# Kernel tuning notes

Measured on AMD Instinct MI355X. Metric: run time of the kernel, lower is better.

The kernel has to match this reference:

```python
import jax, jax.numpy as jnp
import numpy as np

B, AT, NBR = 8, 96, 512
NG, NT = 25, 5            # n_gaussian_triple, n_theta
NANG = NG * NT            # 125, filternet input dim
NF = 128                  # n_filters
NB = 128                  # n_atom_basis


def ssp(x):
    # shifted softplus: ln(0.5*e^x + 0.5) = softplus(x) - ln(2)
    return jax.nn.softplus(x) - jnp.asarray(np.log(2.0), x.dtype)


def setup_inputs() -> dict:
    key = jax.random.key(0)
    ks = jax.random.split(key, 16)
    s = lambda fan_in: 1.0 / np.sqrt(fan_in)
    return {
        "x": jax.random.normal(ks[0], (B, AT, NB), jnp.float32),
        "triple_ijk": jax.random.uniform(ks[1], (B, AT, NBR, NANG), jnp.float32),
        "neighbors_j": jax.random.randint(ks[2], (B, AT, NBR), 0, AT, jnp.int32),
        "neighbors_k": jax.random.randint(ks[3], (B, AT, NBR), 0, AT, jnp.int32),
        "triple_mask": jnp.ones((B, AT, NBR), jnp.float32),
        # filter network (Dense ssp -> Dense linear)
        "W1": jax.random.normal(ks[4], (NANG, NF), jnp.float32) * s(NANG),
        "b1": jnp.zeros((NF,), jnp.float32),
        "W2": jax.random.normal(ks[5], (NF, NF), jnp.float32) * s(NF),
        "b2": jnp.zeros((NF,), jnp.float32),
        # cfconv in2f (no bias) and f2out (ssp activation)
        "Win": jax.random.normal(ks[6], (NB, NF), jnp.float32) * s(NB),
        "Wf2": jax.random.normal(ks[7], (NF, NB), jnp.float32) * s(NF),
        "bf2": jnp.zeros((NB,), jnp.float32),
        # final dense (linear) before residual
        "Wd": jax.random.normal(ks[8], (NB, NB), jnp.float32) * s(NB),
        "bd": jnp.zeros((NB,), jnp.float32),
    }


def _gather_atoms(y, nbh):
    # y: (B, At, F); nbh: (B, At, Nbr) -> (B, At, Nbr, F)
    b, at, nbr = nbh.shape
    idx = nbh.reshape(b, at * nbr, 1)
    return jnp.take_along_axis(y, idx, axis=1).reshape(b, at, nbr, y.shape[-1])


def reference(x, triple_ijk, neighbors_j, neighbors_k, triple_mask,
              W1, b1, W2, b2, Win, Wf2, bf2, Wd, bd):
    # filter network on angular/radial triple features -> (B, At, Nbr, NF)
    W_triple = ssp(triple_ijk @ W1 + b1) @ W2 + b2
    # in2f
    y = x @ Win                                  # (B, At, NF)
    y_j = _gather_atoms(y, neighbors_j)          # (B, At, Nbr, NF)
    y_k = _gather_atoms(y, neighbors_k)          # (B, At, Nbr, NF)
    # element-wise continuous-filter conv over triples, mask padded triples
    yt = y_j * y_k * W_triple * triple_mask[..., None]
    agg = jnp.sum(yt, axis=2)                    # sum-aggregate over triples
    v = ssp(agg @ Wf2 + bf2)                     # f2out with shifted softplus
    v = v @ Wd + bd                              # interaction dense
    return x + v                                 # residual
```

## Files before the change

### kernel.cpp

```cpp
#include <hip/hip_runtime.h>
#include <math.h>

#define B_    8
#define AT_   96
#define NBR_  512
#define NANG_ 125
#define NF_   128
#define NB_   128
#define TN    32
#define NCHUNK 4
#define CROWS (NBR_ / NCHUNK)
#define TSTRIDE 136
#define JSTRIDE 132

typedef __attribute__((ext_vector_type(8))) short bf16x8;
typedef __attribute__((ext_vector_type(4))) float f32x4;
typedef float f32x4u __attribute__((ext_vector_type(4), aligned(4)));
typedef __attribute__((ext_vector_type(4))) unsigned int u32x4;

__device__ __forceinline__ short f2bf(float f) {
    union { float f; unsigned u; } x; x.f = f;
    return (short)((x.u + 0x8000u) >> 16);
}

__device__ __forceinline__ unsigned pk2bf(float a, float b) {
    union { float f; unsigned u; } x, y; x.f = a; y.f = b;
    return ((x.u + 0x8000u) >> 16) | ((y.u + 0x8000u) & 0xffff0000u);
}

__device__ __forceinline__ float sspf(float x) {
    float p = __builtin_amdgcn_exp2f(x * 1.44269504088896340736f);
    float l = __builtin_amdgcn_logf(1.0f + p);
    return 0.69314718055994530942f * l - 0.69314718055994530942f;
}

__global__ __launch_bounds__(128) void prep_kernel(
    const float* __restrict__ x, const float* __restrict__ Win,
    const float* __restrict__ W1, const float* __restrict__ W2,
    float* __restrict__ y, short* __restrict__ w1p, short* __restrict__ w2p)
{
    __shared__ float xs[4][NB_];
    int blk = blockIdx.x, tid = threadIdx.x;
    if (blk < 192) {
        int row0 = blk * 4;
        #pragma unroll
        for (int r = 0; r < 4; r++) xs[r][tid] = x[(row0 + r) * NB_ + tid];
        __syncthreads();
        float a0 = 0.f, a1 = 0.f, a2 = 0.f, a3 = 0.f;
        #pragma unroll 8
        for (int k = 0; k < NB_; k++) {
            float w = Win[k * NF_ + tid];
            a0 = fmaf(xs[0][k], w, a0);
            a1 = fmaf(xs[1][k], w, a1);
            a2 = fmaf(xs[2][k], w, a2);
            a3 = fmaf(xs[3][k], w, a3);
        }
        y[(row0 + 0) * NF_ + tid] = a0;
        y[(row0 + 1) * NF_ + tid] = a1;
        y[(row0 + 2) * NF_ + tid] = a2;
        y[(row0 + 3) * NF_ + tid] = a3;
    } else {
        int t = (blk - 192) * 128 + tid;
        int j = t & 7, lane = (t >> 3) & 63, ks = (t >> 9) & 3, ct = t >> 11;
        int k = ks * 32 + (lane >> 4) * 8 + j;
        int n = ct * 16 + (lane & 15);
        w1p[t] = (k < NANG_) ? f2bf(W1[k * NF_ + n]) : (short)0;
        w2p[t] = f2bf(W2[k * NF_ + n]);
    }
}

__global__ __launch_bounds__(256) void triple_partial(
    const float* __restrict__ trip,
    const int* __restrict__ nbj, const int* __restrict__ nbk,
    const float* __restrict__ maskg,
    const float* __restrict__ b1g, const float* __restrict__ b2g,
    const float* __restrict__ y, const short* __restrict__ w1p,
    const short* __restrict__ w2p, float* __restrict__ pagg)
{
    __shared__ short ts[TN * TSTRIDE];
    __shared__ short hs[TN * TSTRIDE];
    __shared__ float yjk[TN * JSTRIDE];

    const int tid = threadIdx.x;
    const int wave = tid >> 6, lane = tid & 63;
    const int quad = lane >> 4, col = lane & 15;
    const int blk = blockIdx.x;
    const int bid = blk >> 2, c = blk & 3;
    const int b = bid / AT_;

    const float* tpc = trip + (long)bid * NBR_ * NANG_ + (long)c * CROWS * NANG_;
    const int nb_base = bid * NBR_ + c * CROWS;

    const int ct0 = 2 * wave, ct1 = 2 * wave + 1;
    const int f0 = ct0 * 16 + col, f1 = ct1 * 16 + col;
    const float bias1_0 = b1g[f0], bias1_1 = b1g[f1];
    const float bias2_0 = b2g[f0], bias2_1 = b2g[f1];

    const int srow = tid >> 3, schunk = tid & 7;
    const int yrow = tid >> 3, ypart = tid & 7;

    bf16x8 w1f0[4], w1f1[4];
    #pragma unroll
    for (int ks = 0; ks < 4; ks++) {
        w1f0[ks] = *(const bf16x8*)&w1p[(ct0 * 4 + ks) * 512 + lane * 8];
        w1f1[ks] = *(const bf16x8*)&w1p[(ct1 * 4 + ks) * 512 + lane * 8];
    }

    float accw0 = 0.f, accw1 = 0.f;

    for (int nt = 0; nt < CROWS / TN; nt++) {
        const float* tp = tpc + nt * TN * NANG_;
        const int nrow0 = nb_base + nt * TN;

        const float* rowp = tp + srow * NANG_ + schunk * 16;
        f32x4u v0, v1, v2, v3;
        if (schunk < 7) {
            v0 = *(const f32x4u*)(rowp + 0);
            v1 = *(const f32x4u*)(rowp + 4);
            v2 = *(const f32x4u*)(rowp + 8);
            v3 = *(const f32x4u*)(rowp + 12);
        } else {
            v0 = *(const f32x4u*)(rowp + 0);
            v1 = *(const f32x4u*)(rowp + 4);
            v2 = *(const f32x4u*)(rowp + 8);
            v3.x = rowp[12]; v3.y = 0.f; v3.z = 0.f; v3.w = 0.f;
        }

        const int jj = nbj[nrow0 + yrow], kk = nbk[nrow0 + yrow];
        const float m = maskg[nrow0 + yrow];
        const float* yjp = y + (b * AT_ + jj) * NF_ + ypart * 16;
        const float* ykp = y + (b * AT_ + kk) * NF_ + ypart * 16;
        f32x4 j0 = ((const f32x4*)yjp)[0], j1 = ((const f32x4*)yjp)[1];
        f32x4 j2 = ((const f32x4*)yjp)[2], j3 = ((const f32x4*)yjp)[3];
        f32x4 k0 = ((const f32x4*)ykp)[0], k1 = ((const f32x4*)ykp)[1];
        f32x4 k2 = ((const f32x4*)ykp)[2], k3 = ((const f32x4*)ykp)[3];

        __syncthreads();

        {
            u32x4 pA, pB;
            pA.x = pk2bf(v0.x, v0.y); pA.y = pk2bf(v0.z, v0.w);
            pA.z = pk2bf(v1.x, v1.y); pA.w = pk2bf(v1.z, v1.w);
            pB.x = pk2bf(v2.x, v2.y); pB.y = pk2bf(v2.z, v2.w);
            pB.z = pk2bf(v3.x, v3.y); pB.w = pk2bf(v3.z, v3.w);
            u32x4* dst = (u32x4*)&ts[srow * TSTRIDE + schunk * 16];
            dst[0] = pA;
            dst[1] = pB;
        }
        {
            float* d = &yjk[yrow * JSTRIDE + ypart * 16];
            *(f32x4*)(d + 0)  = j0 * k0 * m;
            *(f32x4*)(d + 4)  = j1 * k1 * m;
            *(f32x4*)(d + 8)  = j2 * k2 * m;
            *(f32x4*)(d + 12) = j3 * k3 * m;
        }
        __syncthreads();

        f32x4 d00 = {0,0,0,0}, d01 = {0,0,0,0}, d10 = {0,0,0,0}, d11 = {0,0,0,0};
        #pragma unroll
        for (int ks = 0; ks < 4; ks++) {
            bf16x8 a0 = *(const bf16x8*)&ts[(     col) * TSTRIDE + ks * 32 + quad * 8];
            bf16x8 a1 = *(const bf16x8*)&ts[(16 + col) * TSTRIDE + ks * 32 + quad * 8];
            d00 = __builtin_amdgcn_mfma_f32_16x16x32_bf16(a0, w1f0[ks], d00, 0, 0, 0);
            d01 = __builtin_amdgcn_mfma_f32_16x16x32_bf16(a0, w1f1[ks], d01, 0, 0, 0);
            d10 = __builtin_amdgcn_mfma_f32_16x16x32_bf16(a1, w1f0[ks], d10, 0, 0, 0);
            d11 = __builtin_amdgcn_mfma_f32_16x16x32_bf16(a1, w1f1[ks], d11, 0, 0, 0);
        }
        #pragma unroll
        for (int r = 0; r < 4; r++) {
            int row0 = quad * 4 + r, row1 = 16 + quad * 4 + r;
            hs[row0 * TSTRIDE + f0] = f2bf(sspf(d00[r] + bias1_0));
            hs[row0 * TSTRIDE + f1] = f2bf(sspf(d01[r] + bias1_1));
            hs[row1 * TSTRIDE + f0] = f2bf(sspf(d10[r] + bias1_0));
            hs[row1 * TSTRIDE + f1] = f2bf(sspf(d11[r] + bias1_1));
        }
        __syncthreads();

        f32x4 e00 = {0,0,0,0}, e01 = {0,0,0,0}, e10 = {0,0,0,0}, e11 = {0,0,0,0};
        #pragma unroll
        for (int ks = 0; ks < 4; ks++) {
            bf16x8 a0 = *(const bf16x8*)&hs[(     col) * TSTRIDE + ks * 32 + quad * 8];
            bf16x8 a1 = *(const bf16x8*)&hs[(16 + col) * TSTRIDE + ks * 32 + quad * 8];
            bf16x8 w0 = *(const bf16x8*)&w2p[(ct0 * 4 + ks) * 512 + lane * 8];
            bf16x8 w1 = *(const bf16x8*)&w2p[(ct1 * 4 + ks) * 512 + lane * 8];
            e00 = __builtin_amdgcn_mfma_f32_16x16x32_bf16(a0, w0, e00, 0, 0, 0);
            e01 = __builtin_amdgcn_mfma_f32_16x16x32_bf16(a0, w1, e01, 0, 0, 0);
            e10 = __builtin_amdgcn_mfma_f32_16x16x32_bf16(a1, w0, e10, 0, 0, 0);
            e11 = __builtin_amdgcn_mfma_f32_16x16x32_bf16(a1, w1, e11, 0, 0, 0);
        }
        #pragma unroll
        for (int r = 0; r < 4; r++) {
            int row0 = quad * 4 + r, row1 = 16 + quad * 4 + r;
            accw0 += (e00[r] + bias2_0) * yjk[row0 * JSTRIDE + f0];
            accw1 += (e01[r] + bias2_1) * yjk[row0 * JSTRIDE + f1];
            accw0 += (e10[r] + bias2_0) * yjk[row1 * JSTRIDE + f0];
            accw1 += (e11[r] + bias2_1) * yjk[row1 * JSTRIDE + f1];
        }
    }

    accw0 += __shfl_xor(accw0, 16, 64);
    accw0 += __shfl_xor(accw0, 32, 64);
    accw1 += __shfl_xor(accw1, 16, 64);
    accw1 += __shfl_xor(accw1, 32, 64);
    if (quad == 0) {
        pagg[blk * NF_ + f0] = accw0;
        pagg[blk * NF_ + f1] = accw1;
    }
}

__global__ __launch_bounds__(128) void finish_kernel(
    const float* __restrict__ x, const float* __restrict__ pagg,
    const float* __restrict__ Wf2, const float* __restrict__ bf2,
    const float* __restrict__ Wd, const float* __restrict__ bd,
    float* __restrict__ out)
{
    __shared__ float aggs[NF_];
    __shared__ float t1s[NF_];
    int bid = blockIdx.x, f = threadIdx.x;
    float a = pagg[(bid * 4 + 0) * NF_ + f] + pagg[(bid * 4 + 1) * NF_ + f]
            + pagg[(bid * 4 + 2) * NF_ + f] + pagg[(bid * 4 + 3) * NF_ + f];
    aggs[f] = a;
    __syncthreads();
    float acc = 0.f;
    #pragma unroll 8
    for (int k = 0; k < NF_; k++) acc = fmaf(aggs[k], Wf2[k * NB_ + f], acc);
    t1s[f] = sspf(acc + bf2[f]);
    __syncthreads();
    acc = 0.f;
    #pragma unroll 8
    for (int k = 0; k < NB_; k++) acc = fmaf(t1s[k], Wd[k * NB_ + f], acc);
    out[bid * NB_ + f] = x[bid * NB_ + f] + acc + bd[f];
}

extern "C" void kernel_launch(void* const* d_in, const int* in_sizes, int n_in,
                              void* d_out, int out_size, void* d_ws, size_t ws_size,
                              hipStream_t stream) {
    const float* x    = (const float*)d_in[0];
    const float* trip = (const float*)d_in[1];
    const int*   nbj  = (const int*)d_in[2];
    const int*   nbk  = (const int*)d_in[3];
    const float* mask = (const float*)d_in[4];
    const float* W1   = (const float*)d_in[5];
    const float* b1   = (const float*)d_in[6];
    const float* W2   = (const float*)d_in[7];
    const float* b2   = (const float*)d_in[8];
    const float* Win  = (const float*)d_in[9];
    const float* Wf2  = (const float*)d_in[10];
    const float* bf2  = (const float*)d_in[11];
    const float* Wd   = (const float*)d_in[12];
    const float* bd   = (const float*)d_in[13];
    float* out = (float*)d_out;

    char* ws = (char*)d_ws;
    float* y    = (float*)ws;
    short* w1p  = (short*)(ws + 393216);
    short* w2p  = (short*)(ws + 393216 + 32768);
    float* pagg = (float*)(ws + 393216 + 65536);

    prep_kernel<<<320, 128, 0, stream>>>(x, Win, W1, W2, y, w1p, w2p);
    triple_partial<<<B_ * AT_ * NCHUNK, 256, 0, stream>>>(trip, nbj, nbk, mask,
        b1, b2, y, w1p, w2p, pagg);
    finish_kernel<<<B_ * AT_, 128, 0, stream>>>(x, pagg, Wf2, bf2, Wd, bd, out);
}
```

Baseline: 352.6 us.

## Split triples into 8 chunks, keep W2 fragments in registers, store yjk as bf16

Doubles the number of blocks by splitting each atom's 512 triples into 8 chunks instead of 4, which gives more parallelism across CUs. The W2 MFMA fragments are loaded into registers once instead of being re-read from global memory every tile. The yj*yk*mask product is stored in shared memory as bf16, which cuts LDS footprint so more blocks can be resident. In exchange the kernel uses more registers, the final reduction has more partials to sum, and the bf16 rounding of the gather product costs some precision.

```diff
diff --git a/kernel.cpp b/kernel.cpp
--- a/kernel.cpp
+++ b/kernel.cpp
@@ -8,10 +8,9 @@
 #define NF_   128
 #define NB_   128
 #define TN    32
-#define NCHUNK 4
+#define NCHUNK 8
 #define CROWS (NBR_ / NCHUNK)
 #define TSTRIDE 136
-#define JSTRIDE 132
 
 typedef __attribute__((ext_vector_type(8))) short bf16x8;
 typedef __attribute__((ext_vector_type(4))) float f32x4;
@@ -22,7 +21,10 @@
     union { float f; unsigned u; } x; x.f = f;
     return (short)((x.u + 0x8000u) >> 16);
 }
-
+__device__ __forceinline__ float bf2f(unsigned short h) {
+    union { unsigned u; float f; } x; x.u = ((unsigned)h) << 16;
+    return x.f;
+}
 __device__ __forceinline__ unsigned pk2bf(float a, float b) {
     union { float f; unsigned u; } x, y; x.f = a; y.f = b;
     return ((x.u + 0x8000u) >> 16) | ((y.u + 0x8000u) & 0xffff0000u);
@@ -79,13 +81,13 @@
 {
     __shared__ short ts[TN * TSTRIDE];
     __shared__ short hs[TN * TSTRIDE];
-    __shared__ float yjk[TN * JSTRIDE];
+    __shared__ unsigned short yjkb[TN * TSTRIDE];
 
     const int tid = threadIdx.x;
     const int wave = tid >> 6, lane = tid & 63;
     const int quad = lane >> 4, col = lane & 15;
     const int blk = blockIdx.x;
-    const int bid = blk >> 2, c = blk & 3;
+    const int bid = blk >> 3, c = blk & 7;
     const int b = bid / AT_;
 
     const float* tpc = trip + (long)bid * NBR_ * NANG_ + (long)c * CROWS * NANG_;
@@ -97,13 +99,14 @@
     const float bias2_0 = b2g[f0], bias2_1 = b2g[f1];
 
     const int srow = tid >> 3, schunk = tid & 7;
-    const int yrow = tid >> 3, ypart = tid & 7;
-
-    bf16x8 w1f0[4], w1f1[4];
+
+    bf16x8 w1f0[4], w1f1[4], w2f0[4], w2f1[4];
     #pragma unroll
     for (int ks = 0; ks < 4; ks++) {
         w1f0[ks] = *(const bf16x8*)&w1p[(ct0 * 4 + ks) * 512 + lane * 8];
         w1f1[ks] = *(const bf16x8*)&w1p[(ct1 * 4 + ks) * 512 + lane * 8];
+        w2f0[ks] = *(const bf16x8*)&w2p[(ct0 * 4 + ks) * 512 + lane * 8];
+        w2f1[ks] = *(const bf16x8*)&w2p[(ct1 * 4 + ks) * 512 + lane * 8];
     }
 
     float accw0 = 0.f, accw1 = 0.f;
@@ -126,10 +129,10 @@
             v3.x = rowp[12]; v3.y = 0.f; v3.z = 0.f; v3.w = 0.f;
         }
 
-        const int jj = nbj[nrow0 + yrow], kk = nbk[nrow0 + yrow];
-        const float m = maskg[nrow0 + yrow];
-        const float* yjp = y + (b * AT_ + jj) * NF_ + ypart * 16;
-        const float* ykp = y + (b * AT_ + kk) * NF_ + ypart * 16;
+        const int jj = nbj[nrow0 + srow], kk = nbk[nrow0 + srow];
+        const float m = maskg[nrow0 + srow];
+        const float* yjp = y + (b * AT_ + jj) * NF_ + schunk * 16;
+        const float* ykp = y + (b * AT_ + kk) * NF_ + schunk * 16;
         f32x4 j0 = ((const f32x4*)yjp)[0], j1 = ((const f32x4*)yjp)[1];
         f32x4 j2 = ((const f32x4*)yjp)[2], j3 = ((const f32x4*)yjp)[3];
         f32x4 k0 = ((const f32x4*)ykp)[0], k1 = ((const f32x4*)ykp)[1];
@@ -148,11 +151,16 @@
             dst[1] = pB;
         }
         {
-            float* d = &yjk[yrow * JSTRIDE + ypart * 16];
-            *(f32x4*)(d + 0)  = j0 * k0 * m;
-            *(f32x4*)(d + 4)  = j1 * k1 * m;
-            *(f32x4*)(d + 8)  = j2 * k2 * m;
-            *(f32x4*)(d + 12) = j3 * k3 * m;
+            f32x4 p0 = j0 * k0 * m, p1 = j1 * k1 * m;
+            f32x4 p2 = j2 * k2 * m, p3 = j3 * k3 * m;
+            u32x4 qA, qB;
+            qA.x = pk2bf(p0.x, p0.y); qA.y = pk2bf(p0.z, p0.w);
+            qA.z = pk2bf(p1.x, p1.y); qA.w = pk2bf(p1.z, p1.w);
+            qB.x = pk2bf(p2.x, p2.y); qB.y = pk2bf(p2.z, p2.w);
+            qB.z = pk2bf(p3.x, p3.y); qB.w = pk2bf(p3.z, p3.w);
+            u32x4* dst = (u32x4*)&yjkb[srow * TSTRIDE + schunk * 16];
+            dst[0] = qA;
+            dst[1] = qB;
         }
         __syncthreads();
 
@@ -181,20 +189,18 @@
         for (int ks = 0; ks < 4; ks++) {
             bf16x8 a0 = *(const bf16x8*)&hs[(     col) * TSTRIDE + ks * 32 + quad * 8];
             bf16x8 a1 = *(const bf16x8*)&hs[(16 + col) * TSTRIDE + ks * 32 + quad * 8];
-            bf16x8 w0 = *(const bf16x8*)&w2p[(ct0 * 4 + ks) * 512 + lane * 8];
-            bf16x8 w1 = *(const bf16x8*)&w2p[(ct1 * 4 + ks) * 512 + lane * 8];
-            e00 = __builtin_amdgcn_mfma_f32_16x16x32_bf16(a0, w0, e00, 0, 0, 0);
-            e01 = __builtin_amdgcn_mfma_f32_16x16x32_bf16(a0, w1, e01, 0, 0, 0);
-            e10 = __builtin_amdgcn_mfma_f32_16x16x32_bf16(a1, w0, e10, 0, 0, 0);
-            e11 = __builtin_amdgcn_mfma_f32_16x16x32_bf16(a1, w1, e11, 0, 0, 0);
+            e00 = __builtin_amdgcn_mfma_f32_16x16x32_bf16(a0, w2f0[ks], e00, 0, 0, 0);
+            e01 = __builtin_amdgcn_mfma_f32_16x16x32_bf16(a0, w2f1[ks], e01, 0, 0, 0);
+            e10 = __builtin_amdgcn_mfma_f32_16x16x32_bf16(a1, w2f0[ks], e10, 0, 0, 0);
+            e11 = __builtin_amdgcn_mfma_f32_16x16x32_bf16(a1, w2f1[ks], e11, 0, 0, 0);
         }
         #pragma unroll
         for (int r = 0; r < 4; r++) {
             int row0 = quad * 4 + r, row1 = 16 + quad * 4 + r;
-            accw0 += (e00[r] + bias2_0) * yjk[row0 * JSTRIDE + f0];
-            accw1 += (e01[r] + bias2_1) * yjk[row0 * JSTRIDE + f1];
-            accw0 += (e10[r] + bias2_0) * yjk[row1 * JSTRIDE + f0];
-            accw1 += (e11[r] + bias2_1) * yjk[row1 * JSTRIDE + f1];
+            accw0 += (e00[r] + bias2_0) * bf2f(yjkb[row0 * TSTRIDE + f0]);
+            accw1 += (e01[r] + bias2_1) * bf2f(yjkb[row0 * TSTRIDE + f1]);
+            accw0 += (e10[r] + bias2_0) * bf2f(yjkb[row1 * TSTRIDE + f0]);
+            accw1 += (e11[r] + bias2_1) * bf2f(yjkb[row1 * TSTRIDE + f1]);
         }
     }
 
@@ -217,8 +223,9 @@
     __shared__ float aggs[NF_];
     __shared__ float t1s[NF_];
     int bid = blockIdx.x, f = threadIdx.x;
-    float a = pagg[(bid * 4 + 0) * NF_ + f] + pagg[(bid * 4 + 1) * NF_ + f]
-            + pagg[(bid * 4 + 2) * NF_ + f] + pagg[(bid * 4 + 3) * NF_ + f];
+    float a = 0.f;
+    #pragma unroll
+    for (int c = 0; c < NCHUNK; c++) a += pagg[(bid * NCHUNK + c) * NF_ + f];
     aggs[f] = a;
     __syncthreads();
     float acc = 0.f;
```

Result: no change. 347.3 us (-1.5%).
